# Performance work log

Measured on AMD Instinct MI355X. Metric: run time of the kernel, lower is better.

Reference implementation:

```python
import jax, jax.numpy as jnp
import numpy as np

B, N, C = 4, 2048, 1024
H = 16
D = C // H  # head dim = 64

def setup_inputs() -> dict:
    key = jax.random.key(0)
    k1, k2, k3 = jax.random.split(key, 3)
    x = jax.random.normal(k1, (B, N, C), dtype=jnp.float32)
    w_attn = jax.random.normal(k2, (C, 3 * C), dtype=jnp.float32) * (C ** -0.5)
    w_proj = jax.random.normal(k3, (C, C), dtype=jnp.float32) * (C ** -0.5)
    return {"x": x, "w_attn": w_attn, "w_proj": w_proj}

def reference(x, w_attn, w_proj):
    # fused QKV projection (bias=False)
    qkv = jnp.einsum('bnc,cf->bnf', x, w_attn)            # [B,N,3C]
    q, k, v = jnp.split(qkv, 3, axis=-1)                  # each [B,N,C]
    # [B,H,N,D]
    q = q.reshape(B, N, H, D).transpose(0, 2, 1, 3)
    k = k.reshape(B, N, H, D).transpose(0, 2, 1, 3)
    v = v.reshape(B, N, H, D).transpose(0, 2, 1, 3)
    # scaled dot-product attention, non-causal, no mask, dropout_p=0
    scale = 1.0 / jnp.sqrt(jnp.asarray(D, dtype=q.dtype))
    scores = jnp.einsum('bhqd,bhkd->bhqk', q, k) * scale  # [B,H,N,N]
    attn = jax.nn.softmax(scores, axis=-1)
    y = jnp.einsum('bhqk,bhkd->bhqd', attn, v)            # [B,H,N,D]
    y = y.transpose(0, 2, 1, 3).reshape(B, N, C)
    # output projection (bias=False); resid dropout is identity at p=0
    return jnp.einsum('bnc,co->bno', y, w_proj)
```

## Files before the change

### kernel.cpp

```cpp
#include <hip/hip_runtime.h>
#include <hip/hip_bf16.h>

typedef __hip_bfloat16 bf16;
typedef short short8 __attribute__((ext_vector_type(8)));
typedef float f32x4 __attribute__((ext_vector_type(4)));
typedef float f32x16 __attribute__((ext_vector_type(16)));

#define GLOBAL_AS __attribute__((address_space(1)))
#define LDS_AS __attribute__((address_space(3)))

__device__ inline unsigned short f2bf(float x) {
    union { float f; unsigned u; } v; v.f = x;
    unsigned r = v.u + 0x7fffu + ((v.u >> 16) & 1u);
    return (unsigned short)(r >> 16);
}

__device__ inline unsigned pkbf(float a, float b) {
    float2 f; f.x = a; f.y = b;
    union { __hip_bfloat162 h; unsigned u; } c;
    c.h = __float22bfloat162_rn(f);
    return c.u;
}

__device__ inline float fast_exp2(float x) {
#if __has_builtin(__builtin_amdgcn_exp2f)
    return __builtin_amdgcn_exp2f(x);
#else
    return exp2f(x);
#endif
}

__device__ inline void async16(const void* g, void* l) {
    __builtin_amdgcn_global_load_lds((const GLOBAL_AS void*)g, (LDS_AS void*)l, 16, 0, 0);
}


__global__ __launch_bounds__(256) void cvt_f32_bf16(const float* __restrict__ in,
                                                    unsigned short* __restrict__ out, int n4) {
    int i = blockIdx.x * 256 + threadIdx.x;
    if (i < n4) {
        float4 v = ((const float4*)in)[i];
        ushort4 o;
        o.x = f2bf(v.x); o.y = f2bf(v.y); o.z = f2bf(v.z); o.w = f2bf(v.w);
        ((ushort4*)out)[i] = o;
    }
}

__global__ __launch_bounds__(256) void transpose_bf16(const float* __restrict__ in,
                                                      unsigned short* __restrict__ out,
                                                      int R, int Cc) {
    __shared__ float s[32][33];
    int tx = threadIdx.x & 31, ty = threadIdx.x >> 5;
    int c0 = blockIdx.x * 32, r0 = blockIdx.y * 32;
#pragma unroll
    for (int i = 0; i < 4; i++)
        s[ty + i * 8][tx] = in[(size_t)(r0 + ty + i * 8) * Cc + c0 + tx];
    __syncthreads();
#pragma unroll
    for (int i = 0; i < 4; i++)
        out[(size_t)(c0 + ty + i * 8) * R + r0 + tx] = f2bf(s[tx][ty + i * 8]);
}


template <int MODE>
__global__ __launch_bounds__(256) void gemm_bf16(const bf16* __restrict__ A,
                                                 const bf16* __restrict__ Bt,
                                                 unsigned short* __restrict__ outQ,
                                                 unsigned short* __restrict__ outK,
                                                 unsigned short* __restrict__ outV,
                                                 float* __restrict__ outF, float qscale) {
    const int KD = 1024;
    __shared__ __align__(16) char smem[34816];
    bf16* sA = (bf16*)smem;
    bf16* sB = (bf16*)(smem + 16384);
    const int t = threadIdx.x;
    const int w = t >> 6, lane = t & 63, l15 = lane & 15, qd = lane >> 4;
    const int nbx = gridDim.x;
    const int lid = blockIdx.y * nbx + blockIdx.x;
    const int q8 = (nbx * gridDim.y) >> 3;
    const int sid = (lid & 7) * q8 + (lid >> 3);
    const int bn = sid % nbx, bm = sid / nbx;
    const int wm = (w >> 1) * 64, wn = (w & 1) * 64;
    const int sw = l15 & 7;

    f32x4 acc[4][4];
#pragma unroll
    for (int i = 0; i < 4; i++)
#pragma unroll
        for (int j = 0; j < 4; j++) acc[i][j] = (f32x4){0.f, 0.f, 0.f, 0.f};

    const int rsub = lane >> 3;
    const int csrc = ((lane & 7) ^ rsub) << 3;
    const bf16* Ab = A + (size_t)(bm * 128 + w * 32 + rsub) * KD + csrc;
    const bf16* Bb = Bt + (size_t)(bn * 128 + w * 32 + rsub) * KD + csrc;
    bf16* sAw = sA + (w * 32) * 64;
    bf16* sBw = sB + (w * 32) * 64;

    for (int kt = 0; kt < 16; ++kt) {
#pragma unroll
        for (int j = 0; j < 4; ++j) {
            async16(Ab + (size_t)(j * 8) * KD + kt * 64, sAw + j * 512);
            async16(Bb + (size_t)(j * 8) * KD + kt * 64, sBw + j * 512);
        }
        __syncthreads();
#pragma unroll
        for (int ks = 0; ks < 2; ++ks) {
            const int cphys = (((ks * 4 + qd) ^ sw) << 3);
            short8 af[4], bfv[4];
#pragma unroll
            for (int mi = 0; mi < 4; mi++)
                af[mi] = *(const short8*)&sA[(wm + mi * 16 + l15) * 64 + cphys];
#pragma unroll
            for (int ni = 0; ni < 4; ni++)
                bfv[ni] = *(const short8*)&sB[(wn + ni * 16 + l15) * 64 + cphys];
#pragma unroll
            for (int mi = 0; mi < 4; mi++)
#pragma unroll
                for (int ni = 0; ni < 4; ni++)
                    acc[mi][ni] = __builtin_amdgcn_mfma_f32_16x16x32_bf16(af[mi], bfv[ni],
                                                                          acc[mi][ni], 0, 0, 0);
        }
        __syncthreads();
    }

    if (MODE == 0) {
        unsigned short* sC = (unsigned short*)smem;
        const int part = bn >> 3;
        const int hb = (bn & 7) * 2;
        if (part < 2) {
            const float sc = (part == 0) ? qscale : 1.0f;
            unsigned short* dst = (part == 0) ? outQ : outK;
#pragma unroll
            for (int mi = 0; mi < 4; mi++)
#pragma unroll
                for (int ni = 0; ni < 4; ni++)
#pragma unroll
                    for (int r = 0; r < 4; r++)
                        sC[(wm + mi * 16 + qd * 4 + r) * 136 + wn + ni * 16 + l15] =
                            f2bf(acc[mi][ni][r] * sc);
            __syncthreads();
#pragma unroll
            for (int i = 0; i < 8; i++) {
                const int j = t + i * 256;
                const int row = j >> 4, c16 = j & 15;
                uint4 v = *(const uint4*)&sC[row * 136 + c16 * 8];
                const int m = bm * 128 + row;
                const int b = m >> 11, ns = m & 2047;
                const int h = hb + (c16 >> 3);
                const int dd = (c16 & 7) * 8;
                *(uint4*)&dst[((size_t)(b * 16 + h) * 2048 + ns) * 64 + dd] = v;
            }
        } else {
#pragma unroll
            for (int ni = 0; ni < 4; ni++)
#pragma unroll
                for (int mi = 0; mi < 4; mi++) {
                    uint2 pk;
                    pk.x = (unsigned)f2bf(acc[mi][ni][0]) | ((unsigned)f2bf(acc[mi][ni][1]) << 16);
                    pk.y = (unsigned)f2bf(acc[mi][ni][2]) | ((unsigned)f2bf(acc[mi][ni][3]) << 16);
                    *(uint2*)&sC[(wn + ni * 16 + l15) * 136 + wm + mi * 16 + qd * 4] = pk;
                }
            __syncthreads();
            const int m0b = bm * 128;
            const int b = m0b >> 11, ns0 = m0b & 2047;
#pragma unroll
            for (int i = 0; i < 8; i++) {
                const int j = t + i * 256;
                const int f = j >> 4, tc = j & 15;
                uint4 v = *(const uint4*)&sC[f * 136 + tc * 8];
                const int h = hb + (f >> 6), dd = f & 63;
                *(uint4*)&outV[((size_t)(b * 16 + h) * 64 + dd) * 2048 + ns0 + tc * 8] = v;
            }
        }
    } else {
        float* sF = (float*)smem;
#pragma unroll
        for (int pass = 0; pass < 2; ++pass) {
            if (pass) __syncthreads();
            if ((wm >> 6) == pass) {
#pragma unroll
                for (int mi = 0; mi < 4; mi++)
#pragma unroll
                    for (int ni = 0; ni < 4; ni++)
#pragma unroll
                        for (int r = 0; r < 4; r++)
                            sF[(mi * 16 + qd * 4 + r) * 132 + wn + ni * 16 + l15] =
                                acc[mi][ni][r];
            }
            __syncthreads();
#pragma unroll
            for (int i = 0; i < 8; i++) {
                const int j = t + i * 256;
                const int row = j >> 5, c4 = j & 31;
                float4 v = *(const float4*)&sF[row * 132 + c4 * 4];
                *(float4*)&outF[(size_t)(bm * 128 + pass * 64 + row) * 1024 + bn * 128 +
                                c4 * 4] = v;
            }
        }
    }
}


__global__ __launch_bounds__(256) void attn_kernel(const bf16* __restrict__ Q,
                                                   const bf16* __restrict__ K,
                                                   const bf16* __restrict__ Vt,
                                                   bf16* __restrict__ Y) {
    const int blk = blockIdx.x;
    const int bh = (blk & 7) * 8 + (blk >> 7);
    const int qt = (blk >> 3) & 15;
    const int b = bh >> 4, h16 = bh & 15;
    const int t = threadIdx.x, w = t >> 6, lane = t & 63;
    const int c = lane & 31, hl = lane >> 5;
    const int sw = c & 7;

    __shared__ __align__(16) char smem[32768];
    bf16* sK0 = (bf16*)smem;
    bf16* sK1 = (bf16*)(smem + 8192);
    bf16* sV0 = (bf16*)(smem + 16384);
    bf16* sV1 = (bf16*)(smem + 24576);
    bf16* sO = (bf16*)smem;

    const size_t bhbase = (size_t)bh * 2048 * 64;

    short8 qf[4];
#pragma unroll
    for (int kc = 0; kc < 4; kc++)
        qf[kc] = *(const short8*)(Q + bhbase + (size_t)(qt * 128 + w * 32 + c) * 64 +
                                  kc * 16 + hl * 8);

    f32x16 z16;
#pragma unroll
    for (int i = 0; i < 16; i++) z16[i] = 0.f;
    f32x16 ot[2];
#pragma unroll
    for (int i = 0; i < 16; i++) { ot[0][i] = 0.f; ot[1][i] = 0.f; }
    float l_run = 0.f;

    const int rsub = lane >> 3;
    const int cg = ((lane & 7) ^ rsub) << 3;
    const bf16* Kb = K + bhbase + (size_t)(w * 16 + rsub) * 64 + cg;
    const bf16* Vb = Vt + bhbase + (size_t)(w * 16 + rsub) * 2048 + cg;
    const int ldsoff = (w * 16) * 64;

#define STAGE(ktile, sKb, sVb)                                                      \
    {                                                                               \
        _Pragma("unroll") for (int j = 0; j < 2; j++) {                             \
            async16(Kb + (size_t)(ktile) * 4096 + j * 512, (sKb) + ldsoff + j * 512); \
            async16(Vb + (size_t)(ktile) * 64 + (size_t)j * 16384,                  \
                    (sVb) + ldsoff + j * 512);                                      \
        }                                                                           \
    }

    auto compute = [&](const bf16* __restrict__ sKb, const bf16* __restrict__ sVb) {
#pragma unroll
        for (int kt2 = 0; kt2 < 2; ++kt2) {
            short8 kf0 = *(const short8*)&sKb[(kt2 * 32 + c) * 64 + ((hl ^ sw) << 3)];
            __builtin_amdgcn_s_setprio(1);
            f32x16 accS = __builtin_amdgcn_mfma_f32_32x32x16_bf16(kf0, qf[0], z16, 0, 0, 0);
#pragma unroll
            for (int kc = 1; kc < 4; kc++) {
                short8 kf =
                    *(const short8*)&sKb[(kt2 * 32 + c) * 64 + (((kc * 2 + hl) ^ sw) << 3)];
                accS = __builtin_amdgcn_mfma_f32_32x32x16_bf16(kf, qf[kc], accS, 0, 0, 0);
            }
            __builtin_amdgcn_s_setprio(0);
            unsigned u[8];
            float ls = 0.f;
#pragma unroll
            for (int i = 0; i < 8; i++) {
                float p0 = fast_exp2(accS[2 * i]);
                float p1 = fast_exp2(accS[2 * i + 1]);
                ls += p0 + p1;
                u[i] = pkbf(p0, p1);
            }
            l_run += ls;
            union { uint4 u4; short8 s8; } F[2];
            F[0].u4.x = u[0]; F[0].u4.y = u[1]; F[0].u4.z = u[2]; F[0].u4.w = u[3];
            F[1].u4.x = u[4]; F[1].u4.y = u[5]; F[1].u4.z = u[6]; F[1].u4.w = u[7];
            __builtin_amdgcn_s_setprio(1);
#pragma unroll
            for (int g = 0; g < 2; ++g) {
#pragma unroll
                for (int mi2 = 0; mi2 < 2; mi2++) {
                    const bf16* vr = &sVb[(mi2 * 32 + c) * 64];
                    uint2 a0 = *(const uint2*)&vr[(((kt2 * 4 + 2 * g) ^ sw) << 3) + hl * 4];
                    uint2 a1 =
                        *(const uint2*)&vr[(((kt2 * 4 + 2 * g + 1) ^ sw) << 3) + hl * 4];
                    union { uint4 u4; short8 s8; } vf;
                    vf.u4.x = a0.x; vf.u4.y = a0.y; vf.u4.z = a1.x; vf.u4.w = a1.y;
                    ot[mi2] =
                        __builtin_amdgcn_mfma_f32_32x32x16_bf16(vf.s8, F[g].s8, ot[mi2], 0, 0, 0);
                }
            }
            __builtin_amdgcn_s_setprio(0);
        }
    };

    STAGE(0, sK0, sV0);
    for (int kt = 0; kt < 32; kt += 2) {
        __syncthreads();
        STAGE(kt + 1, sK1, sV1);
        compute(sK0, sV0);
        __syncthreads();
        if (kt + 2 < 32) STAGE(kt + 2, sK0, sV0);
        compute(sK1, sV1);
    }
    __syncthreads();

    float l = l_run + __shfl_xor(l_run, 32, 64);
    float rl = 1.f / l;
#pragma unroll
    for (int mi2 = 0; mi2 < 2; mi2++)
#pragma unroll
        for (int q4 = 0; q4 < 4; q4++) {
            const int d0 = mi2 * 32 + q4 * 8 + hl * 4;
            uint2 pk;
            pk.x = pkbf(ot[mi2][q4 * 4 + 0] * rl, ot[mi2][q4 * 4 + 1] * rl);
            pk.y = pkbf(ot[mi2][q4 * 4 + 2] * rl, ot[mi2][q4 * 4 + 3] * rl);
            *(uint2*)&sO[(w * 32 + c) * 72 + d0] = pk;
        }
    __syncthreads();
#pragma unroll
    for (int i = 0; i < 4; i++) {
        int row = (t >> 3) + i * 32, doff = (t & 7) * 8;
        uint4 vv = *(const uint4*)&sO[row * 72 + doff];
        *(uint4*)(Y + ((size_t)(b * 2048 + qt * 128 + row)) * 1024 + h16 * 64 + doff) = vv;
    }
#undef STAGE
}


extern "C" void kernel_launch(void* const* d_in, const int* in_sizes, int n_in,
                              void* d_out, int out_size, void* d_ws, size_t ws_size,
                              hipStream_t stream) {
    const float* x = (const float*)d_in[0];
    const float* w_attn = (const float*)d_in[1];
    const float* w_proj = (const float*)d_in[2];
    float* out = (float*)d_out;
    char* ws = (char*)d_ws;

    bf16* xb = (bf16*)(ws);
    bf16* waT = (bf16*)(ws + 16777216);
    bf16* wpT = (bf16*)(ws + 23068672);
    bf16* qb = (bf16*)(ws + 25165824);
    bf16* kb = (bf16*)(ws + 41943040);
    bf16* vtb = (bf16*)(ws + 58720256);

    cvt_f32_bf16<<<8192, 256, 0, stream>>>(x, (unsigned short*)xb, 2097152);
    transpose_bf16<<<dim3(96, 32), 256, 0, stream>>>(w_attn, (unsigned short*)waT, 1024, 3072);
    transpose_bf16<<<dim3(32, 32), 256, 0, stream>>>(w_proj, (unsigned short*)wpT, 1024, 1024);

    const float qscale = 0.125f * 1.44269504088896340736f;
    gemm_bf16<0><<<dim3(24, 64), 256, 0, stream>>>(xb, waT, (unsigned short*)qb,
                                                   (unsigned short*)kb, (unsigned short*)vtb,
                                                   nullptr, qscale);
    attn_kernel<<<dim3(1024), 256, 0, stream>>>(qb, kb, vtb, xb );
    gemm_bf16<1><<<dim3(8, 64), 256, 0, stream>>>(xb, wpT, nullptr, nullptr, nullptr, out, 1.0f);
}
```

Before: 285.6 us.

## Double query rows per attention block and drop GEMM tile swizzle

```diff
diff --git a/kernel.cpp b/kernel.cpp
--- a/kernel.cpp
+++ b/kernel.cpp
@@ -75,11 +75,7 @@
     bf16* sB = (bf16*)(smem + 16384);
     const int t = threadIdx.x;
     const int w = t >> 6, lane = t & 63, l15 = lane & 15, qd = lane >> 4;
-    const int nbx = gridDim.x;
-    const int lid = blockIdx.y * nbx + blockIdx.x;
-    const int q8 = (nbx * gridDim.y) >> 3;
-    const int sid = (lid & 7) * q8 + (lid >> 3);
-    const int bn = sid % nbx, bm = sid / nbx;
+    const int bn = blockIdx.x, bm = blockIdx.y;
     const int wm = (w >> 1) * 64, wn = (w & 1) * 64;
     const int sw = l15 & 7;
 
@@ -206,14 +202,14 @@
                                                    const bf16* __restrict__ Vt,
                                                    bf16* __restrict__ Y) {
     const int blk = blockIdx.x;
-    const int bh = (blk & 7) * 8 + (blk >> 7);
-    const int qt = (blk >> 3) & 15;
+    const int bh = (blk & 7) * 8 + (blk >> 6);
+    const int qt = (blk >> 3) & 7;
     const int b = bh >> 4, h16 = bh & 15;
     const int t = threadIdx.x, w = t >> 6, lane = t & 63;
     const int c = lane & 31, hl = lane >> 5;
     const int sw = c & 7;
 
-    __shared__ __align__(16) char smem[32768];
+    __shared__ __align__(16) char smem[36864];
     bf16* sK0 = (bf16*)smem;
     bf16* sK1 = (bf16*)(smem + 8192);
     bf16* sV0 = (bf16*)(smem + 16384);
@@ -222,19 +218,24 @@
 
     const size_t bhbase = (size_t)bh * 2048 * 64;
 
-    short8 qf[4];
-#pragma unroll
-    for (int kc = 0; kc < 4; kc++)
-        qf[kc] = *(const short8*)(Q + bhbase + (size_t)(qt * 128 + w * 32 + c) * 64 +
-                                  kc * 16 + hl * 8);
+    short8 qfA[4], qfB[4];
+#pragma unroll
+    for (int kc = 0; kc < 4; kc++) {
+        qfA[kc] = *(const short8*)(Q + bhbase + (size_t)(qt * 256 + w * 64 + c) * 64 +
+                                   kc * 16 + hl * 8);
+        qfB[kc] = *(const short8*)(Q + bhbase + (size_t)(qt * 256 + w * 64 + 32 + c) * 64 +
+                                   kc * 16 + hl * 8);
+    }
 
     f32x16 z16;
 #pragma unroll
     for (int i = 0; i < 16; i++) z16[i] = 0.f;
-    f32x16 ot[2];
-#pragma unroll
-    for (int i = 0; i < 16; i++) { ot[0][i] = 0.f; ot[1][i] = 0.f; }
-    float l_run = 0.f;
+    f32x16 ot[4];
+#pragma unroll
+    for (int j = 0; j < 4; j++)
+#pragma unroll
+        for (int i = 0; i < 16; i++) ot[j][i] = 0.f;
+    float lA = 0.f, lB = 0.f;
 
     const int rsub = lane >> 3;
     const int cg = ((lane & 7) ^ rsub) << 3;
@@ -254,29 +255,40 @@
     auto compute = [&](const bf16* __restrict__ sKb, const bf16* __restrict__ sVb) {
 #pragma unroll
         for (int kt2 = 0; kt2 < 2; ++kt2) {
-            short8 kf0 = *(const short8*)&sKb[(kt2 * 32 + c) * 64 + ((hl ^ sw) << 3)];
+            short8 kf[4];
+#pragma unroll
+            for (int kc = 0; kc < 4; kc++)
+                kf[kc] =
+                    *(const short8*)&sKb[(kt2 * 32 + c) * 64 + (((kc * 2 + hl) ^ sw) << 3)];
             __builtin_amdgcn_s_setprio(1);
-            f32x16 accS = __builtin_amdgcn_mfma_f32_32x32x16_bf16(kf0, qf[0], z16, 0, 0, 0);
+            f32x16 accA = __builtin_amdgcn_mfma_f32_32x32x16_bf16(kf[0], qfA[0], z16, 0, 0, 0);
+            f32x16 accB = __builtin_amdgcn_mfma_f32_32x32x16_bf16(kf[0], qfB[0], z16, 0, 0, 0);
 #pragma unroll
             for (int kc = 1; kc < 4; kc++) {
-                short8 kf =
-                    *(const short8*)&sKb[(kt2 * 32 + c) * 64 + (((kc * 2 + hl) ^ sw) << 3)];
-                accS = __builtin_amdgcn_mfma_f32_32x32x16_bf16(kf, qf[kc], accS, 0, 0, 0);
+                accA = __builtin_amdgcn_mfma_f32_32x32x16_bf16(kf[kc], qfA[kc], accA, 0, 0, 0);
+                accB = __builtin_amdgcn_mfma_f32_32x32x16_bf16(kf[kc], qfB[kc], accB, 0, 0, 0);
             }
             __builtin_amdgcn_s_setprio(0);
-            unsigned u[8];
-            float ls = 0.f;
+            unsigned uA[8], uB[8];
+            float lsA = 0.f, lsB = 0.f;
 #pragma unroll
             for (int i = 0; i < 8; i++) {
-                float p0 = fast_exp2(accS[2 * i]);
-                float p1 = fast_exp2(accS[2 * i + 1]);
-                ls += p0 + p1;
-                u[i] = pkbf(p0, p1);
-            }
-            l_run += ls;
-            union { uint4 u4; short8 s8; } F[2];
-            F[0].u4.x = u[0]; F[0].u4.y = u[1]; F[0].u4.z = u[2]; F[0].u4.w = u[3];
-            F[1].u4.x = u[4]; F[1].u4.y = u[5]; F[1].u4.z = u[6]; F[1].u4.w = u[7];
+                float a0 = fast_exp2(accA[2 * i]);
+                float a1 = fast_exp2(accA[2 * i + 1]);
+                lsA += a0 + a1;
+                uA[i] = pkbf(a0, a1);
+                float b0 = fast_exp2(accB[2 * i]);
+                float b1 = fast_exp2(accB[2 * i + 1]);
+                lsB += b0 + b1;
+                uB[i] = pkbf(b0, b1);
+            }
+            lA += lsA;
+            lB += lsB;
+            union { uint4 u4; short8 s8; } FA[2], FB[2];
+            FA[0].u4.x = uA[0]; FA[0].u4.y = uA[1]; FA[0].u4.z = uA[2]; FA[0].u4.w = uA[3];
+            FA[1].u4.x = uA[4]; FA[1].u4.y = uA[5]; FA[1].u4.z = uA[6]; FA[1].u4.w = uA[7];
+            FB[0].u4.x = uB[0]; FB[0].u4.y = uB[1]; FB[0].u4.z = uB[2]; FB[0].u4.w = uB[3];
+            FB[1].u4.x = uB[4]; FB[1].u4.y = uB[5]; FB[1].u4.z = uB[6]; FB[1].u4.w = uB[7];
             __builtin_amdgcn_s_setprio(1);
 #pragma unroll
             for (int g = 0; g < 2; ++g) {
@@ -289,7 +301,9 @@
                     union { uint4 u4; short8 s8; } vf;
                     vf.u4.x = a0.x; vf.u4.y = a0.y; vf.u4.z = a1.x; vf.u4.w = a1.y;
                     ot[mi2] =
-                        __builtin_amdgcn_mfma_f32_32x32x16_bf16(vf.s8, F[g].s8, ot[mi2], 0, 0, 0);
+                        __builtin_amdgcn_mfma_f32_32x32x16_bf16(vf.s8, FA[g].s8, ot[mi2], 0, 0, 0);
+                    ot[2 + mi2] = __builtin_amdgcn_mfma_f32_32x32x16_bf16(vf.s8, FB[g].s8,
+                                                                          ot[2 + mi2], 0, 0, 0);
                 }
             }
             __builtin_amdgcn_s_setprio(0);
@@ -307,24 +321,30 @@
     }
     __syncthreads();
 
-    float l = l_run + __shfl_xor(l_run, 32, 64);
-    float rl = 1.f / l;
+    float lAt = lA + __shfl_xor(lA, 32, 64);
+    float lBt = lB + __shfl_xor(lB, 32, 64);
+    float rlA = 1.f / lAt;
+    float rlB = 1.f / lBt;
 #pragma unroll
     for (int mi2 = 0; mi2 < 2; mi2++)
 #pragma unroll
         for (int q4 = 0; q4 < 4; q4++) {
             const int d0 = mi2 * 32 + q4 * 8 + hl * 4;
-            uint2 pk;
-            pk.x = pkbf(ot[mi2][q4 * 4 + 0] * rl, ot[mi2][q4 * 4 + 1] * rl);
-            pk.y = pkbf(ot[mi2][q4 * 4 + 2] * rl, ot[mi2][q4 * 4 + 3] * rl);
-            *(uint2*)&sO[(w * 32 + c) * 72 + d0] = pk;
+            uint2 pkA;
+            pkA.x = pkbf(ot[mi2][q4 * 4 + 0] * rlA, ot[mi2][q4 * 4 + 1] * rlA);
+            pkA.y = pkbf(ot[mi2][q4 * 4 + 2] * rlA, ot[mi2][q4 * 4 + 3] * rlA);
+            *(uint2*)&sO[(w * 64 + c) * 72 + d0] = pkA;
+            uint2 pkB;
+            pkB.x = pkbf(ot[2 + mi2][q4 * 4 + 0] * rlB, ot[2 + mi2][q4 * 4 + 1] * rlB);
+            pkB.y = pkbf(ot[2 + mi2][q4 * 4 + 2] * rlB, ot[2 + mi2][q4 * 4 + 3] * rlB);
+            *(uint2*)&sO[(w * 64 + 32 + c) * 72 + d0] = pkB;
         }
     __syncthreads();
 #pragma unroll
-    for (int i = 0; i < 4; i++) {
+    for (int i = 0; i < 8; i++) {
         int row = (t >> 3) + i * 32, doff = (t & 7) * 8;
         uint4 vv = *(const uint4*)&sO[row * 72 + doff];
-        *(uint4*)(Y + ((size_t)(b * 2048 + qt * 128 + row)) * 1024 + h16 * 64 + doff) = vv;
+        *(uint4*)(Y + ((size_t)(b * 2048 + qt * 256 + row)) * 1024 + h16 * 64 + doff) = vv;
     }
 #undef STAGE
 }
@@ -354,6 +374,6 @@
     gemm_bf16<0><<<dim3(24, 64), 256, 0, stream>>>(xb, waT, (unsigned short*)qb,
                                                    (unsigned short*)kb, (unsigned short*)vtb,
                                                    nullptr, qscale);
-    attn_kernel<<<dim3(1024), 256, 0, stream>>>(qb, kb, vtb, xb );
+    attn_kernel<<<dim3(512), 256, 0, stream>>>(qb, kb, vtb, xb );
     gemm_bf16<1><<<dim3(8, 64), 256, 0, stream>>>(xb, wpT, nullptr, nullptr, nullptr, out, 1.0f);
 }
```

After: 270.0 us, median of 3. -5.5%, faster.
